# Kernel optimization log

Hardware: AMD Instinct MI355X
Metric: run time of the kernel (lower is better)

The kernel has to match this reference:

```python
import jax, jax.numpy as jnp
import numpy as np

N_BUCKET, EPB, K, TAU = 4, 4, 2, 1.0
C, H = 512, 1024
E = N_BUCKET * EPB
B, T = 2, 1024

def _l2norm(v):
    # matches F.normalize(dim=-1): v / max(||v||, 1e-12)
    return v / jnp.maximum(jnp.linalg.norm(v, axis=-1, keepdims=True), 1e-12)

def setup_inputs() -> dict:
    key = jax.random.key(0)
    ks = jax.random.split(key, 8)
    s = 1.0 / np.sqrt(C).astype(np.float32)
    sh = 1.0 / np.sqrt(H).astype(np.float32)
    return {
        "x": jax.random.normal(ks[0], (B, T, C), jnp.float32),
        "op_id": jax.random.randint(ks[1], (B, T), 0, N_BUCKET),
        "expert_key": jax.random.normal(ks[2], (N_BUCKET, EPB, C), jnp.float32) * s,
        "sW1": jax.random.normal(ks[3], (C, H), jnp.float32) * s,
        "sb1": jnp.zeros((H,), jnp.float32),
        "sW2": jax.random.normal(ks[4], (H, C), jnp.float32) * sh,
        "sb2": jnp.zeros((C,), jnp.float32),
        "eW1": jax.random.normal(ks[5], (E, C, H), jnp.float32) * s,
        "eb1": jnp.zeros((E, H), jnp.float32),
        "eW2": jax.random.normal(ks[6], (E, H, C), jnp.float32) * sh,
        "eb2": jnp.zeros((E, C), jnp.float32),
        "gate_logit": jnp.float32(-2.0),
    }

def reference(x, op_id, expert_key, sW1, sb1, sW2, sb2, eW1, eb1, eW2, eb2, gate_logit):
    Bb, Tt, Cc = x.shape
    # --- HierKVRouter ---
    bucket = jnp.clip(op_id, 0, N_BUCKET - 1)                 # (B,T)
    h_n = _l2norm(x)                                          # (B,T,C)
    keys = _l2norm(expert_key)                                # (nb,epb,C)
    keys_bt = keys[bucket]                                    # (B,T,epb,C) gather
    score = jnp.einsum('btc,btec->bte', h_n, keys_bt) / max(TAU, 1e-6)
    probs_local = jax.nn.softmax(score, axis=-1)              # (B,T,epb)
    topv, local = jax.lax.top_k(probs_local, K)               # (B,T,K)
    w = topv / (jnp.sum(topv, axis=-1, keepdims=True) + 1e-9) # combine weights
    gid = bucket[..., None] * EPB + local                     # (B,T,K) global ids
    # --- dispatch / expert MLP / combine ---
    flat_in = jnp.broadcast_to(x[:, :, None, :], (Bb, Tt, K, Cc)).reshape(-1, Cc)
    flat_gid = gid.reshape(-1)                                # (B*T*K,)
    flat_w = w.reshape(-1)                                    # (B*T*K,)
    out = jnp.zeros_like(flat_in)
    for e in range(E):  # fixed small expert count; masked dense = exact math of torch boolean-mask loop
        mask = (flat_gid == e)[:, None]
        h1 = jax.nn.relu(flat_in @ eW1[e] + eb1[e])
        oe = h1 @ eW2[e] + eb2[e]
        out = out + jnp.where(mask, oe * flat_w[:, None], 0.0)
    moe_out = out.reshape(Bb, Tt, K, Cc).sum(axis=2)          # (B,T,C)
    # --- shared dense FFN + gated combine ---
    dense = jax.nn.relu(x @ sW1 + sb1) @ sW2 + sb2
    y = dense + jax.nn.sigmoid(gate_logit) * moe_out
    return y
```

## Files before the change

### kernel.cpp

```cpp
#include <hip/hip_runtime.h>
#include <hip/hip_bf16.h>
#include <math.h>

#define C_DIM 512
#define H_DIM 1024
#define NTOK  2048
#define NSLOT 4096
#define NROWS 6144
#define MAXT128 64
#define MAXT64  112

typedef __attribute__((ext_vector_type(8))) short short8;
typedef __attribute__((ext_vector_type(4))) float floatx4;
typedef __attribute__((address_space(3))) void as3_void;
typedef const __attribute__((address_space(1))) void as1_cvoid;

__device__ __forceinline__ void gload_lds16(const void* g, void* l){
  __builtin_amdgcn_global_load_lds((as1_cvoid*)g, (as3_void*)l, 16, 0, 0);
}

__device__ __forceinline__ unsigned short f2b(float f){
  unsigned int u = __float_as_uint(f);
  unsigned int r = (u + 0x7FFFu + ((u >> 16) & 1u)) >> 16;
  return (unsigned short)r;
}

#define NB_CVT 1024
#define NB_RTR 512
#define NB_T1  1088
#define NB_T2  1088

__global__ __launch_bounds__(256) void k_prep(const float* __restrict__ x,
                                              const int* __restrict__ op_id,
                                              const float* __restrict__ ekey,
                                              const float* __restrict__ sW1,
                                              const float* __restrict__ sW2,
                                              const float* __restrict__ eW1,
                                              const float* __restrict__ eW2,
                                              unsigned short* __restrict__ Xb,
                                              unsigned short* __restrict__ sW1t,
                                              unsigned short* __restrict__ sW2t,
                                              unsigned short* __restrict__ eW1t,
                                              unsigned short* __restrict__ eW2t,
                                              int* __restrict__ gids,
                                              float* __restrict__ wv){
  __shared__ float tile[64 * 129];
  const int bid = blockIdx.x;
  const int tid = threadIdx.x;

  if (bid < NB_CVT){
    int i = bid * 256 + tid;
    float4 v = reinterpret_cast<const float4*>(x)[i];
    ushort4 o;
    o.x = f2b(v.x); o.y = f2b(v.y); o.z = f2b(v.z); o.w = f2b(v.w);
    reinterpret_cast<ushort4*>(Xb)[i] = o;
    return;
  }
  if (bid < NB_CVT + NB_RTR){
    int t = (bid - NB_CVT) * 4 + (tid >> 6);
    int lane = tid & 63;
    const float* xr = x + (size_t)t * C_DIM;
    float xs[8];
    float xn2 = 0.f;
    #pragma unroll
    for (int i = 0; i < 8; i++){ float v = xr[lane + 64*i]; xs[i] = v; xn2 += v*v; }
    #pragma unroll
    for (int o = 32; o; o >>= 1) xn2 += __shfl_xor(xn2, o, 64);
    int bucket = min(max(op_id[t], 0), 3);
    float xn = fmaxf(sqrtf(xn2), 1e-12f);
    float p[4];
    #pragma unroll
    for (int e = 0; e < 4; e++){
      const float* kr = ekey + ((size_t)bucket * 4 + e) * C_DIM;
      float dot = 0.f, kn2 = 0.f;
      #pragma unroll
      for (int i = 0; i < 8; i++){ float kv = kr[lane + 64*i]; dot += xs[i]*kv; kn2 += kv*kv; }
      #pragma unroll
      for (int o = 32; o; o >>= 1){ dot += __shfl_xor(dot, o, 64); kn2 += __shfl_xor(kn2, o, 64); }
      float kn = fmaxf(sqrtf(kn2), 1e-12f);
      p[e] = dot / (xn * kn);
    }
    float mx = fmaxf(fmaxf(p[0], p[1]), fmaxf(p[2], p[3]));
    float Z = 0.f;
    #pragma unroll
    for (int e = 0; e < 4; e++){ p[e] = expf(p[e] - mx); Z += p[e]; }
    #pragma unroll
    for (int e = 0; e < 4; e++) p[e] /= Z;
    int i0 = 0;
    #pragma unroll
    for (int e = 1; e < 4; e++) if (p[e] > p[i0]) i0 = e;
    int i1 = (i0 == 0) ? 1 : 0;
    #pragma unroll
    for (int e = 0; e < 4; e++) if (e != i0 && e != i1 && p[e] > p[i1]) i1 = e;
    float v0 = p[i0], v1 = p[i1];
    float wsum = v0 + v1 + 1e-9f;
    if (lane == 0){
      gids[2*t]   = bucket * 4 + i0;
      gids[2*t+1] = bucket * 4 + i1;
      wv[2*t]   = v0 / wsum;
      wv[2*t+1] = v1 / wsum;
    }
    return;
  }

  const float* in; unsigned short* out;
  int K, N, n0, k0;
  if (bid < NB_CVT + NB_RTR + NB_T1){
    int tb = bid - (NB_CVT + NB_RTR);
    int mat = tb >> 6, tl = tb & 63;
    K = C_DIM; N = H_DIM;
    in  = (mat < 16) ? eW1 + (size_t)mat * K * N : sW1;
    out = (mat < 16) ? eW1t + (size_t)mat * K * N : sW1t;
    n0 = (tl & 15) * 64; k0 = (tl >> 4) * 128;
  } else {
    int tb = bid - (NB_CVT + NB_RTR + NB_T1);
    int mat = tb >> 6, tl = tb & 63;
    K = H_DIM; N = C_DIM;
    in  = (mat < 16) ? eW2 + (size_t)mat * K * N : sW2;
    out = (mat < 16) ? eW2t + (size_t)mat * K * N : sW2t;
    n0 = (tl & 7) * 64; k0 = (tl >> 3) * 128;
  }
  {
    int tx = tid & 15, ty = tid >> 4;
    #pragma unroll
    for (int i = 0; i < 8; i++){
      int k = ty + 16 * i;
      float4 v = *reinterpret_cast<const float4*>(in + (size_t)(k0 + k) * N + n0 + tx * 4);
      tile[(4*tx + 0) * 129 + k] = v.x;
      tile[(4*tx + 1) * 129 + k] = v.y;
      tile[(4*tx + 2) * 129 + k] = v.z;
      tile[(4*tx + 3) * 129 + k] = v.w;
    }
    __syncthreads();
    int wt = tid & 31, wr = tid >> 5;
    #pragma unroll
    for (int i = 0; i < 8; i++){
      int n = wr + 8 * i;
      float4 v = *reinterpret_cast<const float4*>(&tile[n * 129 + 4 * wt]);
      ushort4 o;
      o.x = f2b(v.x); o.y = f2b(v.y); o.z = f2b(v.z); o.w = f2b(v.w);
      *reinterpret_cast<ushort4*>(out + (size_t)(n0 + n) * K + k0 + 4 * wt) = o;
    }
  }
}

__global__ __launch_bounds__(256) void k_sort(const int* __restrict__ gids,
                                              const float* __restrict__ wv,
                                              const float* __restrict__ gate,
                                              int* __restrict__ inv,
                                              int* __restrict__ rowTok,
                                              float* __restrict__ rowW,
                                              int* __restrict__ tiles128,
                                              int* __restrict__ tiles64){
  __shared__ int hist[256][16];
  __shared__ int off[17];
  int t = threadIdx.x;
  float sig = 1.f / (1.f + expf(-gate[0]));
  int h[16];
  #pragma unroll
  for (int e = 0; e < 16; e++) h[e] = 0;
  int base = t * 16;
  for (int s = 0; s < 16; s++){ int g = gids[base + s]; h[g]++; }
  #pragma unroll
  for (int e = 0; e < 16; e++) hist[t][e] = h[e];
  __syncthreads();
  if (t < 16){
    int run = 0;
    for (int i = 0; i < 256; i++){ int v = hist[i][t]; hist[i][t] = run; run += v; }
    off[t + 1] = run;
  }
  __syncthreads();
  if (t == 0){ off[0] = 0; for (int e = 0; e < 16; e++) off[e+1] += off[e]; }
  __syncthreads();
  #pragma unroll
  for (int e = 0; e < 16; e++) h[e] = hist[t][e];
  for (int s = 0; s < 16; s++){
    int slot = base + s;
    int g = gids[slot];
    int pos = off[g] + h[g]; h[g]++;
    inv[slot] = pos;
    rowTok[NTOK + pos] = slot >> 1;
    rowW[NTOK + pos] = sig * wv[slot];
  }
  for (int r = t; r < NTOK; r += 256){ rowTok[r] = r; rowW[r] = 1.0f; }
  __syncthreads();
  if (t == 0){
    int nt = 0;
    for (int r0 = 0; r0 < NTOK; r0 += 128){
      tiles128[nt*3] = r0; tiles128[nt*3+1] = 128; tiles128[nt*3+2] = 16; nt++;
    }
    for (int e = 0; e < 16; e++){
      int c = off[e+1] - off[e];
      for (int r0 = 0; r0 < c; r0 += 128){
        tiles128[nt*3] = NTOK + off[e] + r0;
        tiles128[nt*3+1] = min(128, c - r0);
        tiles128[nt*3+2] = e;
        nt++;
      }
    }
    for (int i = nt; i < MAXT128; i++){ tiles128[i*3] = 0; tiles128[i*3+1] = 0; tiles128[i*3+2] = 0; }
    nt = 0;
    for (int r0 = 0; r0 < NTOK; r0 += 64){
      tiles64[nt*3] = r0; tiles64[nt*3+1] = 64; tiles64[nt*3+2] = 16; nt++;
    }
    for (int e = 0; e < 16; e++){
      int c = off[e+1] - off[e];
      for (int r0 = 0; r0 < c; r0 += 64){
        tiles64[nt*3] = NTOK + off[e] + r0;
        tiles64[nt*3+1] = min(64, c - r0);
        tiles64[nt*3+2] = e;
        nt++;
      }
    }
    for (int i = nt; i < MAXT64; i++){ tiles64[i*3] = 0; tiles64[i*3+1] = 0; tiles64[i*3+2] = 0; }
  }
}

template<int BMT, int KDIM, int NDIM, bool RELU, bool OUTBF, bool WEIGHTED, bool GATHER>
__global__ __launch_bounds__(256) void k_gemm(const unsigned short* __restrict__ A,
                                              const unsigned short* __restrict__ BtE,
                                              const unsigned short* __restrict__ BtS,
                                              const float* __restrict__ biasE,
                                              const float* __restrict__ biasS,
                                              const int* __restrict__ rowTok,
                                              const float* __restrict__ rowW,
                                              const int* __restrict__ tiles,
                                              unsigned short* __restrict__ outB,
                                              float* __restrict__ outF){
  const int tileId = blockIdx.x;
  const int rows = tiles[tileId*3+1];
  if (rows == 0) return;
  const int row0 = tiles[tileId*3];
  const int eid  = tiles[tileId*3+2];
  const unsigned short* Bt = (eid < 16) ? (BtE + (size_t)eid * NDIM * KDIM) : BtS;
  const float* bias = (eid < 16) ? (biasE + eid * NDIM) : biasS;
  const int n0 = blockIdx.y * 128;

  constexpr int MREP = BMT / 32;
  constexpr int AISS = BMT * 8 / 256;
  constexpr int NLD  = AISS + 4;

  __shared__ __align__(16) unsigned short As[2][BMT * 64];
  __shared__ __align__(16) unsigned short Bs[2][128 * 64];

  const int tid = threadIdx.x;
  const int lane = tid & 63;
  const int wid = tid >> 6;
  const int wm = wid >> 1, wn = wid & 1;
  const int l15 = lane & 15, lhi = lane >> 4;

  int aRow[AISS], aOff[AISS];
  #pragma unroll
  for (int j = 0; j < AISS; j++){
    int c = j * 256 + tid;
    int i = c >> 3, op = c & 7;
    int o = op ^ (i & 7);
    int ie = min(i, rows - 1);
    aRow[j] = GATHER ? rowTok[row0 + ie] : (row0 + ie);
    aOff[j] = o * 8;
  }
  int bRow[4], bOff[4];
  #pragma unroll
  for (int j = 0; j < 4; j++){
    int c = j * 256 + tid;
    int i = c >> 3, op = c & 7;
    int o = op ^ (i & 7);
    bRow[j] = n0 + i;
    bOff[j] = o * 8;
  }

  auto STAGE = [&](int buf, int kt){
    #pragma unroll
    for (int j = 0; j < AISS; j++)
      gload_lds16(A + (size_t)aRow[j] * KDIM + kt * 64 + aOff[j],
                  (char*)&As[buf][0] + (j * 256 + tid) * 16);
    #pragma unroll
    for (int j = 0; j < 4; j++)
      gload_lds16(Bt + (size_t)bRow[j] * KDIM + kt * 64 + bOff[j],
                  (char*)&Bs[buf][0] + (j * 256 + tid) * 16);
  };

  floatx4 acc[MREP][4] = {};
  constexpr int NT = KDIM / 64;

  STAGE(0, 0);
  for (int kt = 0; kt < NT; ++kt){
    const int cur = kt & 1;
    if (kt + 1 < NT){
      STAGE(cur ^ 1, kt + 1);
      if constexpr (NLD == 8) asm volatile("s_waitcnt vmcnt(8)" ::: "memory");
      else                    asm volatile("s_waitcnt vmcnt(6)" ::: "memory");
    } else {
      asm volatile("s_waitcnt vmcnt(0)" ::: "memory");
    }
    __builtin_amdgcn_s_barrier();
    asm volatile("" ::: "memory");
    #pragma unroll
    for (int kk = 0; kk < 2; ++kk){
      short8 a[MREP], b[4];
      #pragma unroll
      for (int m = 0; m < MREP; m++){
        int r = wm * (BMT/2) + m * 16 + l15;
        a[m] = *reinterpret_cast<const short8*>(
            (char*)&As[cur][0] + r * 128 + ((kk * 64 + lhi * 16) ^ ((r & 7) << 4)));
      }
      #pragma unroll
      for (int n = 0; n < 4; n++){
        int r = wn * 64 + n * 16 + l15;
        b[n] = *reinterpret_cast<const short8*>(
            (char*)&Bs[cur][0] + r * 128 + ((kk * 64 + lhi * 16) ^ ((r & 7) << 4)));
      }
      #pragma unroll
      for (int m = 0; m < MREP; m++)
        #pragma unroll
        for (int n = 0; n < 4; n++)
          acc[m][n] = __builtin_amdgcn_mfma_f32_16x16x32_bf16(a[m], b[n], acc[m][n], 0, 0, 0);
    }
    asm volatile("" ::: "memory");
    __builtin_amdgcn_s_barrier();
  }

  #pragma unroll
  for (int m = 0; m < MREP; m++){
    #pragma unroll
    for (int n = 0; n < 4; n++){
      int gcol = n0 + wn * 64 + n * 16 + l15;
      float bv = bias[gcol];
      #pragma unroll
      for (int q = 0; q < 4; q++){
        int ri = wm * (BMT/2) + m * 16 + lhi * 4 + q;
        if (ri < rows){
          float v = acc[m][n][q] + bv;
          if constexpr (OUTBF){
            if (RELU) v = fmaxf(v, 0.f);
            outB[(size_t)(row0 + ri) * NDIM + gcol] = f2b(v);
          } else {
            if constexpr (WEIGHTED) v *= rowW[row0 + ri];
            outF[(size_t)(row0 + ri) * NDIM + gcol] = v;
          }
        }
      }
    }
  }
}

__global__ __launch_bounds__(256) void k_combine(const float* __restrict__ O,
                                                 const int* __restrict__ inv,
                                                 float* __restrict__ y){
  int q = blockIdx.x * 256 + threadIdx.x;
  int t = q >> 7, c4 = q & 127;
  const float4* Of = reinterpret_cast<const float4*>(O);
  float4 d  = Of[(size_t)t * 128 + c4];
  int p0 = inv[2*t], p1 = inv[2*t+1];
  float4 o0 = Of[(size_t)(NTOK + p0) * 128 + c4];
  float4 o1 = Of[(size_t)(NTOK + p1) * 128 + c4];
  float4 r;
  r.x = d.x + o0.x + o1.x;
  r.y = d.y + o0.y + o1.y;
  r.z = d.z + o0.z + o1.z;
  r.w = d.w + o0.w + o1.w;
  reinterpret_cast<float4*>(y)[q] = r;
}

extern "C" void kernel_launch(void* const* d_in, const int* in_sizes, int n_in,
                              void* d_out, int out_size, void* d_ws, size_t ws_size,
                              hipStream_t stream){
  const float* x    = (const float*)d_in[0];
  const int*   opid = (const int*)d_in[1];
  const float* ekey = (const float*)d_in[2];
  const float* sW1  = (const float*)d_in[3];
  const float* sb1  = (const float*)d_in[4];
  const float* sW2  = (const float*)d_in[5];
  const float* sb2  = (const float*)d_in[6];
  const float* eW1  = (const float*)d_in[7];
  const float* eb1  = (const float*)d_in[8];
  const float* eW2  = (const float*)d_in[9];
  const float* eb2  = (const float*)d_in[10];
  const float* gate = (const float*)d_in[11];
  float* y = (float*)d_out;

  char* ws = (char*)d_ws;
  size_t off = 0;
  auto alloc = [&](size_t bytes) -> char* {
    char* p = ws + off; off += (bytes + 255) & ~(size_t)255; return p;
  };
  unsigned short* Xb   = (unsigned short*)alloc((size_t)NTOK * C_DIM * 2);
  unsigned short* sW1t = (unsigned short*)alloc((size_t)H_DIM * C_DIM * 2);
  unsigned short* sW2t = (unsigned short*)alloc((size_t)C_DIM * H_DIM * 2);
  unsigned short* eW1t = (unsigned short*)alloc((size_t)16 * H_DIM * C_DIM * 2);
  unsigned short* eW2t = (unsigned short*)alloc((size_t)16 * C_DIM * H_DIM * 2);
  unsigned short* H1   = (unsigned short*)alloc((size_t)NROWS * H_DIM * 2);
  float* O      = (float*)alloc((size_t)NROWS * C_DIM * 4);
  float* wv     = (float*)alloc((size_t)NSLOT * 4);
  int*   gids   = (int*)alloc((size_t)NSLOT * 4);
  int*   inv    = (int*)alloc((size_t)NSLOT * 4);
  int*   rowTok = (int*)alloc((size_t)NROWS * 4);
  float* rowW   = (float*)alloc((size_t)NROWS * 4);
  int*   tiles128 = (int*)alloc((size_t)MAXT128 * 3 * 4);
  int*   tiles64  = (int*)alloc((size_t)MAXT64 * 3 * 4);

  k_prep<<<NB_CVT + NB_RTR + NB_T1 + NB_T2, 256, 0, stream>>>(
      x, opid, ekey, sW1, sW2, eW1, eW2, Xb, sW1t, sW2t, eW1t, eW2t, gids, wv);
  k_sort<<<1, 256, 0, stream>>>(gids, wv, gate, inv, rowTok, rowW, tiles128, tiles64);
  k_gemm<128, C_DIM, H_DIM, true,  true,  false, true ><<<dim3(MAXT128, H_DIM/128), 256, 0, stream>>>(
      Xb, eW1t, sW1t, eb1, sb1, rowTok, rowW, tiles128, H1, nullptr);
  k_gemm<64,  H_DIM, C_DIM, false, false, true,  false><<<dim3(MAXT64, C_DIM/128), 256, 0, stream>>>(
      H1, eW2t, sW2t, eb2, sb2, rowTok, rowW, tiles64, nullptr, O);
  k_combine<<<1024, 256, 0, stream>>>(O, inv, y);
}
```

Before: 82.77 us.

## Overlap weight transposes with sort and GEMM1 by co-scheduling kernels

Splits the monolithic prep kernel so the router (with fused bf16 cast of x) runs first. The single-block sort now shares a launch with the W1 transposes, and the W2 transposes share a launch with the first GEMM. The serial sort and the weight conversion can then hide behind other work instead of running back to back. The sort's serial column scan is also replaced by a parallel Hillis-Steele prefix scan. The cost is more branching per launch and a larger LDS footprint in the fused GEMM1 kernel, which may reduce occupancy.

```diff
diff --git a/kernel.cpp b/kernel.cpp
--- a/kernel.cpp
+++ b/kernel.cpp
@@ -9,6 +9,7 @@
 #define NROWS 6144
 #define MAXT128 64
 #define MAXT64  112
+#define NBG1 512
 
 typedef __attribute__((ext_vector_type(8))) short short8;
 typedef __attribute__((ext_vector_type(4))) float floatx4;
@@ -25,208 +26,329 @@
   return (unsigned short)r;
 }
 
-#define NB_CVT 1024
-#define NB_RTR 512
-#define NB_T1  1088
-#define NB_T2  1088
-
-__global__ __launch_bounds__(256) void k_prep(const float* __restrict__ x,
-                                              const int* __restrict__ op_id,
-                                              const float* __restrict__ ekey,
-                                              const float* __restrict__ sW1,
-                                              const float* __restrict__ sW2,
-                                              const float* __restrict__ eW1,
-                                              const float* __restrict__ eW2,
-                                              unsigned short* __restrict__ Xb,
-                                              unsigned short* __restrict__ sW1t,
-                                              unsigned short* __restrict__ sW2t,
-                                              unsigned short* __restrict__ eW1t,
-                                              unsigned short* __restrict__ eW2t,
-                                              int* __restrict__ gids,
-                                              float* __restrict__ wv){
-  __shared__ float tile[64 * 129];
+__device__ __forceinline__ void transpose_tile(const float* __restrict__ in,
+                                               unsigned short* __restrict__ out,
+                                               int K, int N, int n0, int k0,
+                                               int tid, float* tile){
+  int tx = tid & 15, ty = tid >> 4;
+  #pragma unroll
+  for (int i = 0; i < 8; i++){
+    int k = ty + 16 * i;
+    float4 v = *reinterpret_cast<const float4*>(in + (size_t)(k0 + k) * N + n0 + tx * 4);
+    tile[(4*tx + 0) * 129 + k] = v.x;
+    tile[(4*tx + 1) * 129 + k] = v.y;
+    tile[(4*tx + 2) * 129 + k] = v.z;
+    tile[(4*tx + 3) * 129 + k] = v.w;
+  }
+  __syncthreads();
+  int wt = tid & 31, wr = tid >> 5;
+  #pragma unroll
+  for (int i = 0; i < 8; i++){
+    int n = wr + 8 * i;
+    float4 v = *reinterpret_cast<const float4*>(&tile[n * 129 + 4 * wt]);
+    ushort4 o;
+    o.x = f2b(v.x); o.y = f2b(v.y); o.z = f2b(v.z); o.w = f2b(v.w);
+    *reinterpret_cast<ushort4*>(out + (size_t)(n0 + n) * K + k0 + 4 * wt) = o;
+  }
+}
+
+__global__ __launch_bounds__(256) void k_router(const float* __restrict__ x,
+                                                const int* __restrict__ op_id,
+                                                const float* __restrict__ ekey,
+                                                unsigned short* __restrict__ Xb,
+                                                int* __restrict__ gids,
+                                                float* __restrict__ wv){
+  int t = blockIdx.x * 4 + (threadIdx.x >> 6);
+  int lane = threadIdx.x & 63;
+  const float* xr = x + (size_t)t * C_DIM;
+
+  {
+    const float4* xr4 = reinterpret_cast<const float4*>(xr);
+    float4 a = xr4[lane * 2], b = xr4[lane * 2 + 1];
+    short8 o;
+    o[0] = (short)f2b(a.x); o[1] = (short)f2b(a.y); o[2] = (short)f2b(a.z); o[3] = (short)f2b(a.w);
+    o[4] = (short)f2b(b.x); o[5] = (short)f2b(b.y); o[6] = (short)f2b(b.z); o[7] = (short)f2b(b.w);
+    *reinterpret_cast<short8*>(Xb + (size_t)t * C_DIM + lane * 8) = o;
+  }
+
+  float xs[8];
+  float xn2 = 0.f;
+  #pragma unroll
+  for (int i = 0; i < 8; i++){ float v = xr[lane + 64*i]; xs[i] = v; xn2 += v*v; }
+  #pragma unroll
+  for (int o = 32; o; o >>= 1) xn2 += __shfl_xor(xn2, o, 64);
+  int bucket = min(max(op_id[t], 0), 3);
+  float xn = fmaxf(sqrtf(xn2), 1e-12f);
+  float p[4];
+  #pragma unroll
+  for (int e = 0; e < 4; e++){
+    const float* kr = ekey + ((size_t)bucket * 4 + e) * C_DIM;
+    float dot = 0.f, kn2 = 0.f;
+    #pragma unroll
+    for (int i = 0; i < 8; i++){ float kv = kr[lane + 64*i]; dot += xs[i]*kv; kn2 += kv*kv; }
+    #pragma unroll
+    for (int o = 32; o; o >>= 1){ dot += __shfl_xor(dot, o, 64); kn2 += __shfl_xor(kn2, o, 64); }
+    float kn = fmaxf(sqrtf(kn2), 1e-12f);
+    p[e] = dot / (xn * kn);
+  }
+  float mx = fmaxf(fmaxf(p[0], p[1]), fmaxf(p[2], p[3]));
+  float Z = 0.f;
+  #pragma unroll
+  for (int e = 0; e < 4; e++){ p[e] = expf(p[e] - mx); Z += p[e]; }
+  #pragma unroll
+  for (int e = 0; e < 4; e++) p[e] /= Z;
+  int i0 = 0;
+  #pragma unroll
+  for (int e = 1; e < 4; e++) if (p[e] > p[i0]) i0 = e;
+  int i1 = (i0 == 0) ? 1 : 0;
+  #pragma unroll
+  for (int e = 0; e < 4; e++) if (e != i0 && e != i1 && p[e] > p[i1]) i1 = e;
+  float v0 = p[i0], v1 = p[i1];
+  float wsum = v0 + v1 + 1e-9f;
+  if (lane == 0){
+    gids[2*t]   = bucket * 4 + i0;
+    gids[2*t+1] = bucket * 4 + i1;
+    wv[2*t]   = v0 / wsum;
+    wv[2*t+1] = v1 / wsum;
+  }
+}
+
+__global__ __launch_bounds__(256) void k_sortw1(const int* __restrict__ gids,
+                                                const float* __restrict__ wv,
+                                                const float* __restrict__ gate,
+                                                const float* __restrict__ sW1,
+                                                const float* __restrict__ eW1,
+                                                unsigned short* __restrict__ sW1t,
+                                                unsigned short* __restrict__ eW1t,
+                                                int* __restrict__ inv,
+                                                int* __restrict__ rowTok,
+                                                float* __restrict__ rowW,
+                                                int* __restrict__ tiles128,
+                                                int* __restrict__ tiles64){
+  __shared__ __align__(16) char smem[33280];
   const int bid = blockIdx.x;
   const int tid = threadIdx.x;
 
-  if (bid < NB_CVT){
-    int i = bid * 256 + tid;
-    float4 v = reinterpret_cast<const float4*>(x)[i];
-    ushort4 o;
-    o.x = f2b(v.x); o.y = f2b(v.y); o.z = f2b(v.z); o.w = f2b(v.w);
-    reinterpret_cast<ushort4*>(Xb)[i] = o;
+  if (bid == 0){
+    int (*hist)[16] = (int(*)[16])smem;
+    int* off = (int*)(smem + 16384);
+    float sig = 1.f / (1.f + expf(-gate[0]));
+    int h[16], g_[16];
+    #pragma unroll
+    for (int e = 0; e < 16; e++) h[e] = 0;
+    int base = tid * 16;
+    #pragma unroll
+    for (int s = 0; s < 16; s++){ g_[s] = gids[base + s]; h[g_[s]]++; }
+    #pragma unroll
+    for (int e = 0; e < 16; e++) hist[tid][e] = h[e];
+    __syncthreads();
+    for (int d = 1; d < 256; d <<= 1){
+      int v[16];
+      if (tid >= d){
+        #pragma unroll
+        for (int e = 0; e < 16; e++) v[e] = hist[tid - d][e];
+      }
+      __syncthreads();
+      if (tid >= d){
+        #pragma unroll
+        for (int e = 0; e < 16; e++) hist[tid][e] += v[e];
+      }
+      __syncthreads();
+    }
+    if (tid == 0){
+      off[0] = 0;
+      for (int e = 0; e < 16; e++) off[e+1] = off[e] + hist[255][e];
+    }
+    __syncthreads();
+    int c[16];
+    #pragma unroll
+    for (int e = 0; e < 16; e++) c[e] = off[e] + hist[tid][e] - h[e];
+    #pragma unroll
+    for (int s = 0; s < 16; s++){
+      int slot = base + s;
+      int g = g_[s];
+      int pos = c[g]++;
+      inv[slot] = pos;
+      rowTok[NTOK + pos] = slot >> 1;
+      rowW[NTOK + pos] = sig * wv[slot];
+    }
+    for (int r = tid; r < NTOK; r += 256){ rowTok[r] = r; rowW[r] = 1.0f; }
+    __syncthreads();
+    if (tid == 0){
+      int nt = 0;
+      for (int r0 = 0; r0 < NTOK; r0 += 128){
+        tiles128[nt*3] = r0; tiles128[nt*3+1] = 128; tiles128[nt*3+2] = 16; nt++;
+      }
+      for (int e = 0; e < 16; e++){
+        int cc = off[e+1] - off[e];
+        for (int r0 = 0; r0 < cc; r0 += 128){
+          tiles128[nt*3] = NTOK + off[e] + r0;
+          tiles128[nt*3+1] = min(128, cc - r0);
+          tiles128[nt*3+2] = e;
+          nt++;
+        }
+      }
+      for (int i = nt; i < MAXT128; i++){ tiles128[i*3] = 0; tiles128[i*3+1] = 0; tiles128[i*3+2] = 0; }
+      nt = 0;
+      for (int r0 = 0; r0 < NTOK; r0 += 64){
+        tiles64[nt*3] = r0; tiles64[nt*3+1] = 64; tiles64[nt*3+2] = 16; nt++;
+      }
+      for (int e = 0; e < 16; e++){
+        int cc = off[e+1] - off[e];
+        for (int r0 = 0; r0 < cc; r0 += 64){
+          tiles64[nt*3] = NTOK + off[e] + r0;
+          tiles64[nt*3+1] = min(64, cc - r0);
+          tiles64[nt*3+2] = e;
+          nt++;
+        }
+      }
+      for (int i = nt; i < MAXT64; i++){ tiles64[i*3] = 0; tiles64[i*3+1] = 0; tiles64[i*3+2] = 0; }
+    }
     return;
   }
-  if (bid < NB_CVT + NB_RTR){
-    int t = (bid - NB_CVT) * 4 + (tid >> 6);
-    int lane = tid & 63;
-    const float* xr = x + (size_t)t * C_DIM;
-    float xs[8];
-    float xn2 = 0.f;
-    #pragma unroll
-    for (int i = 0; i < 8; i++){ float v = xr[lane + 64*i]; xs[i] = v; xn2 += v*v; }
-    #pragma unroll
-    for (int o = 32; o; o >>= 1) xn2 += __shfl_xor(xn2, o, 64);
-    int bucket = min(max(op_id[t], 0), 3);
-    float xn = fmaxf(sqrtf(xn2), 1e-12f);
-    float p[4];
-    #pragma unroll
-    for (int e = 0; e < 4; e++){
-      const float* kr = ekey + ((size_t)bucket * 4 + e) * C_DIM;
-      float dot = 0.f, kn2 = 0.f;
-      #pragma unroll
-      for (int i = 0; i < 8; i++){ float kv = kr[lane + 64*i]; dot += xs[i]*kv; kn2 += kv*kv; }
-      #pragma unroll
-      for (int o = 32; o; o >>= 1){ dot += __shfl_xor(dot, o, 64); kn2 += __shfl_xor(kn2, o, 64); }
-      float kn = fmaxf(sqrtf(kn2), 1e-12f);
-      p[e] = dot / (xn * kn);
-    }
-    float mx = fmaxf(fmaxf(p[0], p[1]), fmaxf(p[2], p[3]));
-    float Z = 0.f;
-    #pragma unroll
-    for (int e = 0; e < 4; e++){ p[e] = expf(p[e] - mx); Z += p[e]; }
-    #pragma unroll
-    for (int e = 0; e < 4; e++) p[e] /= Z;
-    int i0 = 0;
-    #pragma unroll
-    for (int e = 1; e < 4; e++) if (p[e] > p[i0]) i0 = e;
-    int i1 = (i0 == 0) ? 1 : 0;
-    #pragma unroll
-    for (int e = 0; e < 4; e++) if (e != i0 && e != i1 && p[e] > p[i1]) i1 = e;
-    float v0 = p[i0], v1 = p[i1];
-    float wsum = v0 + v1 + 1e-9f;
-    if (lane == 0){
-      gids[2*t]   = bucket * 4 + i0;
-      gids[2*t+1] = bucket * 4 + i1;
-      wv[2*t]   = v0 / wsum;
-      wv[2*t+1] = v1 / wsum;
-    }
-    return;
-  }
-
-  const float* in; unsigned short* out;
-  int K, N, n0, k0;
-  if (bid < NB_CVT + NB_RTR + NB_T1){
-    int tb = bid - (NB_CVT + NB_RTR);
-    int mat = tb >> 6, tl = tb & 63;
-    K = C_DIM; N = H_DIM;
-    in  = (mat < 16) ? eW1 + (size_t)mat * K * N : sW1;
-    out = (mat < 16) ? eW1t + (size_t)mat * K * N : sW1t;
-    n0 = (tl & 15) * 64; k0 = (tl >> 4) * 128;
-  } else {
-    int tb = bid - (NB_CVT + NB_RTR + NB_T1);
-    int mat = tb >> 6, tl = tb & 63;
-    K = H_DIM; N = C_DIM;
-    in  = (mat < 16) ? eW2 + (size_t)mat * K * N : sW2;
-    out = (mat < 16) ? eW2t + (size_t)mat * K * N : sW2t;
-    n0 = (tl & 7) * 64; k0 = (tl >> 3) * 128;
-  }
-  {
-    int tx = tid & 15, ty = tid >> 4;
-    #pragma unroll
-    for (int i = 0; i < 8; i++){
-      int k = ty + 16 * i;
-      float4 v = *reinterpret_cast<const float4*>(in + (size_t)(k0 + k) * N + n0 + tx * 4);
-      tile[(4*tx + 0) * 129 + k] = v.x;
-      tile[(4*tx + 1) * 129 + k] = v.y;
-      tile[(4*tx + 2) * 129 + k] = v.z;
-      tile[(4*tx + 3) * 129 + k] = v.w;
-    }
-    __syncthreads();
-    int wt = tid & 31, wr = tid >> 5;
-    #pragma unroll
-    for (int i = 0; i < 8; i++){
-      int n = wr + 8 * i;
-      float4 v = *reinterpret_cast<const float4*>(&tile[n * 129 + 4 * wt]);
-      ushort4 o;
-      o.x = f2b(v.x); o.y = f2b(v.y); o.z = f2b(v.z); o.w = f2b(v.w);
-      *reinterpret_cast<ushort4*>(out + (size_t)(n0 + n) * K + k0 + 4 * wt) = o;
-    }
-  }
-}
-
-__global__ __launch_bounds__(256) void k_sort(const int* __restrict__ gids,
-                                              const float* __restrict__ wv,
-                                              const float* __restrict__ gate,
-                                              int* __restrict__ inv,
-                                              int* __restrict__ rowTok,
-                                              float* __restrict__ rowW,
-                                              int* __restrict__ tiles128,
-                                              int* __restrict__ tiles64){
-  __shared__ int hist[256][16];
-  __shared__ int off[17];
-  int t = threadIdx.x;
-  float sig = 1.f / (1.f + expf(-gate[0]));
-  int h[16];
-  #pragma unroll
-  for (int e = 0; e < 16; e++) h[e] = 0;
-  int base = t * 16;
-  for (int s = 0; s < 16; s++){ int g = gids[base + s]; h[g]++; }
-  #pragma unroll
-  for (int e = 0; e < 16; e++) hist[t][e] = h[e];
-  __syncthreads();
-  if (t < 16){
-    int run = 0;
-    for (int i = 0; i < 256; i++){ int v = hist[i][t]; hist[i][t] = run; run += v; }
-    off[t + 1] = run;
-  }
-  __syncthreads();
-  if (t == 0){ off[0] = 0; for (int e = 0; e < 16; e++) off[e+1] += off[e]; }
-  __syncthreads();
-  #pragma unroll
-  for (int e = 0; e < 16; e++) h[e] = hist[t][e];
-  for (int s = 0; s < 16; s++){
-    int slot = base + s;
-    int g = gids[slot];
-    int pos = off[g] + h[g]; h[g]++;
-    inv[slot] = pos;
-    rowTok[NTOK + pos] = slot >> 1;
-    rowW[NTOK + pos] = sig * wv[slot];
-  }
-  for (int r = t; r < NTOK; r += 256){ rowTok[r] = r; rowW[r] = 1.0f; }
-  __syncthreads();
-  if (t == 0){
-    int nt = 0;
-    for (int r0 = 0; r0 < NTOK; r0 += 128){
-      tiles128[nt*3] = r0; tiles128[nt*3+1] = 128; tiles128[nt*3+2] = 16; nt++;
-    }
-    for (int e = 0; e < 16; e++){
-      int c = off[e+1] - off[e];
-      for (int r0 = 0; r0 < c; r0 += 128){
-        tiles128[nt*3] = NTOK + off[e] + r0;
-        tiles128[nt*3+1] = min(128, c - r0);
-        tiles128[nt*3+2] = e;
-        nt++;
-      }
-    }
-    for (int i = nt; i < MAXT128; i++){ tiles128[i*3] = 0; tiles128[i*3+1] = 0; tiles128[i*3+2] = 0; }
-    nt = 0;
-    for (int r0 = 0; r0 < NTOK; r0 += 64){
-      tiles64[nt*3] = r0; tiles64[nt*3+1] = 64; tiles64[nt*3+2] = 16; nt++;
-    }
-    for (int e = 0; e < 16; e++){
-      int c = off[e+1] - off[e];
-      for (int r0 = 0; r0 < c; r0 += 64){
-        tiles64[nt*3] = NTOK + off[e] + r0;
-        tiles64[nt*3+1] = min(64, c - r0);
-        tiles64[nt*3+2] = e;
-        nt++;
-      }
-    }
-    for (int i = nt; i < MAXT64; i++){ tiles64[i*3] = 0; tiles64[i*3+1] = 0; tiles64[i*3+2] = 0; }
-  }
-}
-
-template<int BMT, int KDIM, int NDIM, bool RELU, bool OUTBF, bool WEIGHTED, bool GATHER>
-__global__ __launch_bounds__(256) void k_gemm(const unsigned short* __restrict__ A,
+
+  int tb = bid - 1;
+  int mat = tb >> 6, tl = tb & 63;
+  const float* in  = (mat < 16) ? eW1 + (size_t)mat * C_DIM * H_DIM : sW1;
+  unsigned short* out = (mat < 16) ? eW1t + (size_t)mat * C_DIM * H_DIM : sW1t;
+  int n0 = (tl & 15) * 64, k0 = (tl >> 4) * 128;
+  transpose_tile(in, out, C_DIM, H_DIM, n0, k0, tid, (float*)smem);
+}
+
+__global__ __launch_bounds__(256) void k_g1w2(const unsigned short* __restrict__ A,
                                               const unsigned short* __restrict__ BtE,
                                               const unsigned short* __restrict__ BtS,
                                               const float* __restrict__ biasE,
                                               const float* __restrict__ biasS,
                                               const int* __restrict__ rowTok,
-                                              const float* __restrict__ rowW,
                                               const int* __restrict__ tiles,
                                               unsigned short* __restrict__ outB,
-                                              float* __restrict__ outF){
+                                              const float* __restrict__ sW2,
+                                              const float* __restrict__ eW2,
+                                              unsigned short* __restrict__ sW2t,
+                                              unsigned short* __restrict__ eW2t){
+  __shared__ __align__(16) char smem[65536];
+  const int bx = blockIdx.x;
+  const int tid = threadIdx.x;
+
+  if (bx >= NBG1){
+    int tb = bx - NBG1;
+    int mat = tb >> 6, tl = tb & 63;
+    const float* in  = (mat < 16) ? eW2 + (size_t)mat * H_DIM * C_DIM : sW2;
+    unsigned short* out = (mat < 16) ? eW2t + (size_t)mat * H_DIM * C_DIM : sW2t;
+    int n0 = (tl & 7) * 64, k0 = (tl >> 3) * 128;
+    transpose_tile(in, out, H_DIM, C_DIM, n0, k0, tid, (float*)smem);
+    return;
+  }
+
+  constexpr int KDIM = C_DIM, NDIM = H_DIM;
+  const int tileId = bx >> 3;
+  const int rows = tiles[tileId*3+1];
+  if (rows == 0) return;
+  const int row0 = tiles[tileId*3];
+  const int eid  = tiles[tileId*3+2];
+  const unsigned short* Bt = (eid < 16) ? (BtE + (size_t)eid * NDIM * KDIM) : BtS;
+  const float* bias = (eid < 16) ? (biasE + eid * NDIM) : biasS;
+  const int n0 = (bx & 7) * 128;
+
+  unsigned short (*As)[128*64] = (unsigned short(*)[128*64])smem;
+  unsigned short (*Bs)[128*64] = (unsigned short(*)[128*64])(smem + 32768);
+
+  const int lane = tid & 63;
+  const int wid = tid >> 6;
+  const int wm = wid >> 1, wn = wid & 1;
+  const int l15 = lane & 15, lhi = lane >> 4;
+
+  int aRow[4], aOff[4], bRow[4], bOff[4];
+  #pragma unroll
+  for (int j = 0; j < 4; j++){
+    int c = j * 256 + tid;
+    int i = c >> 3, op = c & 7;
+    int o = op ^ (i & 7);
+    int ie = min(i, rows - 1);
+    aRow[j] = rowTok[row0 + ie];
+    aOff[j] = o * 8;
+    bRow[j] = n0 + i;
+    bOff[j] = o * 8;
+  }
+
+  auto STAGE = [&](int buf, int kt){
+    #pragma unroll
+    for (int j = 0; j < 4; j++)
+      gload_lds16(A + (size_t)aRow[j] * KDIM + kt * 64 + aOff[j],
+                  (char*)&As[buf][0] + (j * 256 + tid) * 16);
+    #pragma unroll
+    for (int j = 0; j < 4; j++)
+      gload_lds16(Bt + (size_t)bRow[j] * KDIM + kt * 64 + bOff[j],
+                  (char*)&Bs[buf][0] + (j * 256 + tid) * 16);
+  };
+
+  floatx4 acc[4][4] = {};
+  constexpr int NT = KDIM / 64;
+
+  STAGE(0, 0);
+  for (int kt = 0; kt < NT; ++kt){
+    const int cur = kt & 1;
+    if (kt + 1 < NT){
+      STAGE(cur ^ 1, kt + 1);
+      asm volatile("s_waitcnt vmcnt(8)" ::: "memory");
+    } else {
+      asm volatile("s_waitcnt vmcnt(0)" ::: "memory");
+    }
+    __builtin_amdgcn_s_barrier();
+    asm volatile("" ::: "memory");
+    #pragma unroll
+    for (int kk = 0; kk < 2; ++kk){
+      short8 a[4], b[4];
+      #pragma unroll
+      for (int m = 0; m < 4; m++){
+        int r = wm * 64 + m * 16 + l15;
+        a[m] = *reinterpret_cast<const short8*>(
+            (char*)&As[cur][0] + r * 128 + ((kk * 64 + lhi * 16) ^ ((r & 7) << 4)));
+      }
+      #pragma unroll
+      for (int n = 0; n < 4; n++){
+        int r = wn * 64 + n * 16 + l15;
+        b[n] = *reinterpret_cast<const short8*>(
+            (char*)&Bs[cur][0] + r * 128 + ((kk * 64 + lhi * 16) ^ ((r & 7) << 4)));
+      }
+      #pragma unroll
+      for (int m = 0; m < 4; m++)
+        #pragma unroll
+        for (int n = 0; n < 4; n++)
+          acc[m][n] = __builtin_amdgcn_mfma_f32_16x16x32_bf16(a[m], b[n], acc[m][n], 0, 0, 0);
+    }
+    asm volatile("" ::: "memory");
+    __builtin_amdgcn_s_barrier();
+  }
+
+  #pragma unroll
+  for (int m = 0; m < 4; m++){
+    #pragma unroll
+    for (int n = 0; n < 4; n++){
+      int gcol = n0 + wn * 64 + n * 16 + l15;
+      float bv = bias[gcol];
+      #pragma unroll
+      for (int q = 0; q < 4; q++){
+        int ri = wm * 64 + m * 16 + lhi * 4 + q;
+        if (ri < rows){
+          float v = fmaxf(acc[m][n][q] + bv, 0.f);
+          outB[(size_t)(row0 + ri) * NDIM + gcol] = f2b(v);
+        }
+      }
+    }
+  }
+}
+
+template<int BMT, int KDIM, int NDIM>
+__global__ __launch_bounds__(256) void k_gemm2(const unsigned short* __restrict__ A,
+                                               const unsigned short* __restrict__ BtE,
+                                               const unsigned short* __restrict__ BtS,
+                                               const float* __restrict__ biasE,
+                                               const float* __restrict__ biasS,
+                                               const float* __restrict__ rowW,
+                                               const int* __restrict__ tiles,
+                                               float* __restrict__ outF){
   const int tileId = blockIdx.x;
   const int rows = tiles[tileId*3+1];
   if (rows == 0) return;
@@ -238,7 +360,6 @@
 
   constexpr int MREP = BMT / 32;
   constexpr int AISS = BMT * 8 / 256;
-  constexpr int NLD  = AISS + 4;
 
   __shared__ __align__(16) unsigned short As[2][BMT * 64];
   __shared__ __align__(16) unsigned short Bs[2][128 * 64];
@@ -256,7 +377,7 @@
     int i = c >> 3, op = c & 7;
     int o = op ^ (i & 7);
     int ie = min(i, rows - 1);
-    aRow[j] = GATHER ? rowTok[row0 + ie] : (row0 + ie);
+    aRow[j] = row0 + ie;
     aOff[j] = o * 8;
   }
   int bRow[4], bOff[4];
@@ -288,8 +409,7 @@
     const int cur = kt & 1;
     if (kt + 1 < NT){
       STAGE(cur ^ 1, kt + 1);
-      if constexpr (NLD == 8) asm volatile("s_waitcnt vmcnt(8)" ::: "memory");
-      else                    asm volatile("s_waitcnt vmcnt(6)" ::: "memory");
+      asm volatile("s_waitcnt vmcnt(6)" ::: "memory");
     } else {
       asm volatile("s_waitcnt vmcnt(0)" ::: "memory");
     }
@@ -330,14 +450,8 @@
       for (int q = 0; q < 4; q++){
         int ri = wm * (BMT/2) + m * 16 + lhi * 4 + q;
         if (ri < rows){
-          float v = acc[m][n][q] + bv;
-          if constexpr (OUTBF){
-            if (RELU) v = fmaxf(v, 0.f);
-            outB[(size_t)(row0 + ri) * NDIM + gcol] = f2b(v);
-          } else {
-            if constexpr (WEIGHTED) v *= rowW[row0 + ri];
-            outF[(size_t)(row0 + ri) * NDIM + gcol] = v;
-          }
+          float v = (acc[m][n][q] + bv) * rowW[row0 + ri];
+          outF[(size_t)(row0 + ri) * NDIM + gcol] = v;
         }
       }
     }
@@ -399,12 +513,12 @@
   int*   tiles128 = (int*)alloc((size_t)MAXT128 * 3 * 4);
   int*   tiles64  = (int*)alloc((size_t)MAXT64 * 3 * 4);
 
-  k_prep<<<NB_CVT + NB_RTR + NB_T1 + NB_T2, 256, 0, stream>>>(
-      x, opid, ekey, sW1, sW2, eW1, eW2, Xb, sW1t, sW2t, eW1t, eW2t, gids, wv);
-  k_sort<<<1, 256, 0, stream>>>(gids, wv, gate, inv, rowTok, rowW, tiles128, tiles64);
-  k_gemm<128, C_DIM, H_DIM, true,  true,  false, true ><<<dim3(MAXT128, H_DIM/128), 256, 0, stream>>>(
-      Xb, eW1t, sW1t, eb1, sb1, rowTok, rowW, tiles128, H1, nullptr);
-  k_gemm<64,  H_DIM, C_DIM, false, false, true,  false><<<dim3(MAXT64, C_DIM/128), 256, 0, stream>>>(
-      H1, eW2t, sW2t, eb2, sb2, rowTok, rowW, tiles64, nullptr, O);
+  k_router<<<512, 256, 0, stream>>>(x, opid, ekey, Xb, gids, wv);
+  k_sortw1<<<1 + 1088, 256, 0, stream>>>(gids, wv, gate, sW1, eW1, sW1t, eW1t,
+                                         inv, rowTok, rowW, tiles128, tiles64);
+  k_g1w2<<<NBG1 + 1088, 256, 0, stream>>>(Xb, eW1t, sW1t, eb1, sb1, rowTok, tiles128, H1,
+                                          sW2, eW2, sW2t, eW2t);
+  k_gemm2<64, H_DIM, C_DIM><<<dim3(MAXT64, C_DIM/128), 256, 0, stream>>>(
+      H1, eW2t, sW2t, eb2, sb2, rowW, tiles64, O);
   k_combine<<<1024, 256, 0, stream>>>(O, inv, y);
 }
```

New measurement: 79.29 us. 1.04x faster.
